# Kernel optimization log

Measured on AMD Instinct MI355X. Metric: run time of the kernel, lower is better.

Reference implementation:

```python
import jax, jax.numpy as jnp
import numpy as np

EPS = 1e-5
C_M = 256
C_Z = 128
C_H = 32  # hardcoded c_hidden in the module


def rms_norm(x, weight, eps=EPS):
    # x * rsqrt(mean(x^2) + eps) * weight over last axis
    ms = jnp.mean(jnp.square(x), axis=-1, keepdims=True)
    return x * jax.lax.rsqrt(ms + eps) * weight


def setup_inputs() -> dict:
    key = jax.random.key(0)
    ks = jax.random.split(key, 8)
    B, S = 256, 384
    m = jax.random.normal(ks[0], (B, S, C_M), dtype=jnp.float32)
    g_in = jnp.ones((C_M,), dtype=jnp.float32)
    Wq = jax.random.normal(ks[1], (C_M, C_H), dtype=jnp.float32) / np.sqrt(C_M)
    bq = jnp.zeros((C_H,), dtype=jnp.float32)
    Wk = jax.random.normal(ks[2], (C_M, C_H), dtype=jnp.float32) / np.sqrt(C_M)
    bk = jnp.zeros((C_H,), dtype=jnp.float32)
    # init='final' means zero-init in AF-style code, but use small random so grads flow
    Wo = jax.random.normal(ks[3], (C_H * C_H, C_Z), dtype=jnp.float32) * 0.02
    bo = jnp.zeros((C_Z,), dtype=jnp.float32)
    g_out = jnp.ones((C_Z,), dtype=jnp.float32)
    return {"m": m, "g_in": g_in, "Wq": Wq, "bq": bq, "Wk": Wk, "bk": bk,
            "Wo": Wo, "bo": bo, "g_out": g_out}


def reference(m, g_in, Wq, bq, Wk, bk, Wo, bo, g_out):
    B, S, _ = m.shape
    m_norm = rms_norm(m, g_in)                       # [B,S,c_m]
    q = m_norm @ Wq + bq                             # [B,S,c_h]
    k = m_norm @ Wk + bk                             # [B,S,c_h]
    # einsum 'bic,bjd->ijcd': sum over MSA depth b
    outer = jnp.einsum('bic,bjd->ijcd', q, k).reshape(S, S, C_H * C_H)
    z = outer @ Wo + bo                              # [S,S,c_z]
    z = rms_norm(z, g_out)
    return z.astype(jnp.float32)
```

## Files before the change

kernel.cpp:

```cpp
#include <hip/hip_runtime.h>
#include <hip/hip_bf16.h>
#include <stdint.h>

#define S   384
#define CM  256
#define CH  32
#define CZ  128
#define BB  256
#define EPS 1e-5f

typedef __attribute__((ext_vector_type(8))) short bf16x8;
typedef __attribute__((ext_vector_type(4))) float f32x4;

#define OFF_QT    0u
#define OFF_KT    6291456u
#define OFF_WT    (OFF_KT + 6291456u)
#define OFF_WOT   (OFF_WT + 32768u)

__device__ __forceinline__ unsigned short f2bf(float x) {
  union { __hip_bfloat16 h; unsigned short u; } v;
  v.h = __float2bfloat16(x);
  return v.u;
}

__device__ __forceinline__ void gload_lds16(const void* g, char* smem, uint32_t lds_off_uniform) {
  uint32_t l32 = (uint32_t)(uintptr_t)(smem + lds_off_uniform);
  __builtin_amdgcn_global_load_lds(
      (const __attribute__((address_space(1))) uint32_t*)(uintptr_t)g,
      (__attribute__((address_space(3))) uint32_t*)(uintptr_t)l32,
      16, 0, 0);
}

__device__ __forceinline__ int olds_off(int ij, int blk) {
  int slot = (blk & ~7) | (((blk & 7) ^ ((blk >> 3) & 7) ^ (ij & 7)) & 7);
  return ij * 2048 + slot * 16;
}

__global__ void k0_prep(const float* __restrict__ Wq, const float* __restrict__ Wk,
                        const float* __restrict__ Wo,
                        unsigned short* __restrict__ WTg, unsigned short* __restrict__ WoTg) {
  int idx = blockIdx.x * 256 + threadIdx.x;
  if (idx < 64 * 256) {
    int c = idx >> 8, t = idx & 255;
    float v = (c < 32) ? Wq[t * 32 + c] : Wk[t * 32 + (c - 32)];
    WTg[c * 256 + t] = f2bf(v);
  }
  int j = idx - 64 * 256;
  if (j >= 0 && j < 128 * 1024) {
    int e = j >> 10, dc = j & 1023;
    int c = dc & 31, d = dc >> 5;
    WoTg[e * 1024 + dc] = f2bf(Wo[(c * 32 + d) * 128 + e]);
  }
}

__global__ __launch_bounds__(256, 2) void k2_proj(const float* __restrict__ m,
                                                  const float* __restrict__ gin,
                                                  const unsigned short* __restrict__ WTg,
                                                  const float* __restrict__ bq,
                                                  const float* __restrict__ bk,
                                                  unsigned short* __restrict__ qT,
                                                  unsigned short* __restrict__ kT) {
  __shared__ char smem[49664 + 18432] __attribute__((aligned(16)));
  const int tid = threadIdx.x;
  const int w = tid >> 6, lane = tid & 63;
  const int mlo = lane & 15, quad = lane >> 4;
  const int i0 = blockIdx.x * 4, b0 = blockIdx.y * 32;
  float* scl = (float*)(smem + 49152);

  #pragma unroll
  for (int s = 0; s < 8; ++s) {
    int C0 = (w * 8 + s) * 2;
    int c = C0 + (lane >> 5);
    int j = lane & 31;
    int t8 = (j & ~7) | ((j & 7) ^ (c & 7));
    gload_lds16(WTg + c * 256 + t8 * 8, smem, 16384u + (uint32_t)C0 * 512u);
  }

  const int rowA = tid >> 1, halfA = tid & 1;
  const int growA = (b0 + (rowA >> 2)) * S + i0 + (rowA & 3);
  {
    const float4* p = (const float4*)(m + (size_t)growA * CM + halfA * 128);
    float ss = 0.f;
    #pragma unroll 8
    for (int q4 = 0; q4 < 32; ++q4) {
      float4 x = p[q4];
      ss += x.x * x.x + x.y * x.y + x.z * x.z + x.w * x.w;
    }
    ss += __shfl_xor(ss, 1, 64);
    if (!halfA) scl[rowA] = rsqrtf(ss * (1.f / 256.f) + EPS);
  }

  f32x4 acc[2][4];
  #pragma unroll
  for (int p = 0; p < 2; ++p)
    #pragma unroll
    for (int q = 0; q < 4; ++q) acc[p][q] = (f32x4)0.f;

  for (int kb = 0; kb < 4; ++kb) {
    __syncthreads();
    {
      const int row = tid >> 1, tk0 = (tid & 1) * 32;
      const float4* pB = (const float4*)(m + (size_t)growA * CM + kb * 64 + tk0);
      const float4* pG = (const float4*)(gin + kb * 64 + tk0);
      float sc = scl[row];
      #pragma unroll
      for (int u = 0; u < 4; ++u) {
        float4 x0 = pB[u * 2], x1 = pB[u * 2 + 1];
        float4 g0 = pG[u * 2], g1 = pG[u * 2 + 1];
        union { unsigned short h[8]; int4 q; } pk;
        pk.h[0] = f2bf(x0.x * sc * g0.x); pk.h[1] = f2bf(x0.y * sc * g0.y);
        pk.h[2] = f2bf(x0.z * sc * g0.z); pk.h[3] = f2bf(x0.w * sc * g0.w);
        pk.h[4] = f2bf(x1.x * sc * g1.x); pk.h[5] = f2bf(x1.y * sc * g1.y);
        pk.h[6] = f2bf(x1.z * sc * g1.z); pk.h[7] = f2bf(x1.w * sc * g1.w);
        int blkid = (((tid & 1) * 4 + u) ^ (row & 7));
        *(int4*)(smem + row * 128 + blkid * 16) = pk.q;
      }
    }
    __syncthreads();
    #pragma unroll
    for (int ks = 0; ks < 2; ++ks) {
      bf16x8 af[2], bfr[4];
      int k8 = ks * 4 + quad;
      #pragma unroll
      for (int fm = 0; fm < 2; ++fm) {
        int mm = w * 32 + fm * 16 + mlo;
        af[fm] = *(const bf16x8*)(smem + mm * 128 + ((k8 ^ (mm & 7)) * 16));
      }
      #pragma unroll
      for (int fn = 0; fn < 4; ++fn) {
        int c = fn * 16 + mlo;
        int t8 = kb * 8 + ks * 4 + quad;
        bfr[fn] = *(const bf16x8*)(smem + 16384 + c * 512 + (((t8 & ~7) | ((t8 & 7) ^ (c & 7))) * 16));
      }
      #pragma unroll
      for (int fm = 0; fm < 2; ++fm)
        #pragma unroll
        for (int fn = 0; fn < 4; ++fn)
          acc[fm][fn] = __builtin_amdgcn_mfma_f32_16x16x32_bf16(af[fm], bfr[fn], acc[fm][fn], 0, 0, 0);
    }
  }
  __syncthreads();
  unsigned short* Cl = (unsigned short*)(smem + 49664);
  #pragma unroll
  for (int fm = 0; fm < 2; ++fm)
    #pragma unroll
    for (int fn = 0; fn < 4; ++fn) {
      int cc = fn * 16 + mlo;
      float bias = (cc < 32) ? bq[cc] : bk[cc - 32];
      #pragma unroll
      for (int r = 0; r < 4; ++r) {
        int rr = w * 32 + fm * 16 + quad * 4 + r;
        Cl[rr * 72 + cc] = f2bf(acc[fm][fn][r] + bias);
      }
    }
  __syncthreads();
  {
    int il = tid >> 6, cc = tid & 63;
    unsigned short* dst = (cc < 32) ? (qT + ((i0 + il) * 32 + cc) * BB + b0)
                                    : (kT + ((i0 + il) * 32 + (cc - 32)) * BB + b0);
    #pragma unroll
    for (int v = 0; v < 4; ++v) {
      union { unsigned short h[8]; int4 q; } u;
      #pragma unroll
      for (int x = 0; x < 8; ++x) u.h[x] = Cl[((v * 8 + x) * 4 + il) * 72 + cc];
      *(int4*)(dst + v * 8) = u.q;
    }
  }
}

__global__ __launch_bounds__(512, 2) void k3_fused(const unsigned short* __restrict__ qT,
                                                   const unsigned short* __restrict__ kT,
                                                   const unsigned short* __restrict__ WoTp,
                                                   const float* __restrict__ bo,
                                                   const float* __restrict__ gout,
                                                   float* __restrict__ out) {
  __shared__ char smem[65536] __attribute__((aligned(16)));
  const int tid = threadIdx.x;
  const int w = tid >> 6, lane = tid & 63;
  const int wm = w & 3, wn = w >> 2;
  const int mlo = lane & 15, quad = lane >> 4;

  const int bid = blockIdx.x;
  const int xcd = bid & 7, idx = bid >> 3;
  const int ti = idx / 12;
  const int tj = xcd * 12 + (idx % 12);

  f32x4 acc[4][4];
  #pragma unroll
  for (int p = 0; p < 4; ++p)
    #pragma unroll
    for (int q = 0; q < 4; ++q) acc[p][q] = (f32x4)0.f;

  auto stageA = [&](int kb) {
    #pragma unroll
    for (int s = 0; s < 4; ++s) {
      int r = w * 32 + s * 8 + (lane >> 3);
      int k8 = (lane & 7) ^ (r & 7);
      gload_lds16(qT + (ti * 256 + r) * BB + kb * 64 + k8 * 8, smem, (uint32_t)(w * 32 + s * 8) * 128u);
    }
  };
  auto stageB = [&](int kb, int bsel) {
    #pragma unroll
    for (int s = 0; s < 2; ++s) {
      int r = w * 16 + s * 8 + (lane >> 3);
      int k8 = (lane & 7) ^ (r & 7);
      gload_lds16(kT + (tj * 128 + r) * BB + kb * 64 + k8 * 8, smem,
                  32768u + (uint32_t)bsel * 16384u + (uint32_t)(w * 16 + s * 8) * 128u);
    }
  };

  stageA(0); stageB(0, 0);
  __syncthreads();

  for (int kb = 0; kb < 4; ++kb) {
    const int bsel = kb & 1;
    bf16x8 af2[2][4];
    #pragma unroll
    for (int ks = 0; ks < 2; ++ks)
      #pragma unroll
      for (int f = 0; f < 4; ++f) {
        int k8 = ks * 4 + quad;
        int mm = wm * 64 + f * 16 + mlo;
        af2[ks][f] = *(const bf16x8*)(smem + mm * 128 + ((k8 ^ (mm & 7)) * 16));
      }
    __syncthreads();
    if (kb < 3) { stageA(kb + 1); stageB(kb + 1, bsel ^ 1); }
    #pragma unroll
    for (int ks = 0; ks < 2; ++ks) {
      bf16x8 bfr[4];
      int k8 = ks * 4 + quad;
      #pragma unroll
      for (int f = 0; f < 4; ++f) {
        int nn = wn * 64 + f * 16 + mlo;
        bfr[f] = *(const bf16x8*)(smem + 32768 + bsel * 16384 + nn * 128 + ((k8 ^ (nn & 7)) * 16));
      }
      #pragma unroll
      for (int fm = 0; fm < 4; ++fm)
        #pragma unroll
        for (int fn = 0; fn < 4; ++fn)
          acc[fm][fn] = __builtin_amdgcn_mfma_f32_16x16x32_bf16(af2[ks][fm], bfr[fn], acc[fm][fn], 0, 0, 0);
    }
    __syncthreads();
  }

  #pragma unroll
  for (int fm = 0; fm < 4; ++fm)
    #pragma unroll
    for (int fn = 0; fn < 4; ++fn) {
      int col = wn * 64 + fn * 16 + mlo;
      int row0 = wm * 64 + fm * 16 + quad * 4;
      int ij = (row0 >> 5) * 4 + (col >> 5);
      int k20 = (col & 31) * 32 + (row0 & 31);
      int blk = k20 >> 3;
      int off = olds_off(ij, blk) + (k20 & 7) * 2;
      union { unsigned short h[4]; uint2 u; } pk;
      #pragma unroll
      for (int r = 0; r < 4; ++r) pk.h[r] = f2bf(acc[fm][fn][r]);
      *(uint2*)(smem + off) = pk.u;
    }
  __syncthreads();

  const int eg = w >> 1, kh = w & 1;
  const int e0 = eg * 32;
  f32x4 acc2[2][2];
  #pragma unroll
  for (int p = 0; p < 2; ++p)
    #pragma unroll
    for (int q = 0; q < 2; ++q) acc2[p][q] = (f32x4)0.f;

  #pragma unroll 4
  for (int s = 0; s < 16; ++s) {
    int kk = kh * 16 + s;
    int k = kk * 32 + quad * 8;
    int blk = kk * 4 + quad;
    bf16x8 b[2];
    #pragma unroll
    for (int fe = 0; fe < 2; ++fe)
      b[fe] = *(const bf16x8*)(WoTp + (size_t)(e0 + fe * 16 + mlo) * 1024 + k);
    #pragma unroll
    for (int fij = 0; fij < 2; ++fij) {
      int ij = fij * 16 + mlo;
      bf16x8 a = *(const bf16x8*)(smem + olds_off(ij, blk));
      #pragma unroll
      for (int fe = 0; fe < 2; ++fe)
        acc2[fij][fe] = __builtin_amdgcn_mfma_f32_16x16x32_bf16(a, b[fe], acc2[fij][fe], 0, 0, 0);
    }
  }
  __syncthreads();

  float* partf = (float*)smem;
  float* red   = (float*)(smem + 16896);
  float* sclp  = (float*)(smem + 17408);
  if (kh == 1) {
    #pragma unroll
    for (int fij = 0; fij < 2; ++fij)
      #pragma unroll
      for (int fe = 0; fe < 2; ++fe)
        #pragma unroll
        for (int r = 0; r < 4; ++r)
          partf[eg * 1056 + (fij * 16 + quad * 4 + r) * 33 + fe * 16 + mlo] = acc2[fij][fe][r];
  }
  __syncthreads();

  float v[2][2][4];
  if (kh == 0) {
    float bv[2], gv[2];
    #pragma unroll
    for (int fe = 0; fe < 2; ++fe) { bv[fe] = bo[e0 + fe * 16 + mlo]; gv[fe] = gout[e0 + fe * 16 + mlo]; }
    float sq[2][4];
    #pragma unroll
    for (int fij = 0; fij < 2; ++fij)
      #pragma unroll
      for (int r = 0; r < 4; ++r) {
        float t = 0.f;
        #pragma unroll
        for (int fe = 0; fe < 2; ++fe) {
          float x = acc2[fij][fe][r] + partf[eg * 1056 + (fij * 16 + quad * 4 + r) * 33 + fe * 16 + mlo] + bv[fe];
          v[fij][fe][r] = x * gv[fe];
          t += x * x;
        }
        sq[fij][r] = t;
      }
    #pragma unroll
    for (int o = 1; o < 16; o <<= 1)
      #pragma unroll
      for (int fij = 0; fij < 2; ++fij)
        #pragma unroll
        for (int r = 0; r < 4; ++r) sq[fij][r] += __shfl_xor(sq[fij][r], o, 64);
    if (mlo == 0) {
      #pragma unroll
      for (int fij = 0; fij < 2; ++fij)
        #pragma unroll
        for (int r = 0; r < 4; ++r) red[(fij * 16 + quad * 4 + r) * 4 + eg] = sq[fij][r];
    }
  }
  __syncthreads();
  if (tid < 32) {
    float t = red[tid * 4] + red[tid * 4 + 1] + red[tid * 4 + 2] + red[tid * 4 + 3];
    sclp[tid] = rsqrtf(t * (1.f / 128.f) + EPS);
  }
  __syncthreads();
  if (kh == 0) {
    #pragma unroll
    for (int fij = 0; fij < 2; ++fij)
      #pragma unroll
      for (int r = 0; r < 4; ++r) {
        int ij = fij * 16 + quad * 4 + r;
        float sc = sclp[ij];
        int gi = ti * 8 + (ij >> 2), gj = tj * 4 + (ij & 3);
        #pragma unroll
        for (int fe = 0; fe < 2; ++fe)
          out[((size_t)gi * S + gj) * CZ + e0 + fe * 16 + mlo] = v[fij][fe][r] * sc;
      }
  }
}

extern "C" void kernel_launch(void* const* d_in, const int* in_sizes, int n_in,
                              void* d_out, int out_size, void* d_ws, size_t ws_size,
                              hipStream_t stream) {
  const float* m    = (const float*)d_in[0];
  const float* gin  = (const float*)d_in[1];
  const float* Wq   = (const float*)d_in[2];
  const float* bq   = (const float*)d_in[3];
  const float* Wk   = (const float*)d_in[4];
  const float* bk   = (const float*)d_in[5];
  const float* Wo   = (const float*)d_in[6];
  const float* bo   = (const float*)d_in[7];
  const float* gout = (const float*)d_in[8];

  char* ws = (char*)d_ws;
  unsigned short* qT    = (unsigned short*)(ws + OFF_QT);
  unsigned short* kT    = (unsigned short*)(ws + OFF_KT);
  unsigned short* WTg   = (unsigned short*)(ws + OFF_WT);
  unsigned short* WoTp  = (unsigned short*)(ws + OFF_WOT);
  float* out = (float*)d_out;

  hipLaunchKernelGGL(k0_prep, dim3(576), dim3(256), 0, stream, Wq, Wk, Wo, WTg, WoTp);
  hipLaunchKernelGGL(k2_proj, dim3(96, 8), dim3(256), 0, stream, m, gin, WTg, bq, bk, qT, kT);
  hipLaunchKernelGGL(k3_fused, dim3(4608), dim3(512), 0, stream, qT, kT, WoTp, bo, gout, out);
}
```

Baseline: 433.6 us.

## Raise occupancy bounds, reuse LDS for projection output, reorder fused MMA loop

The projection kernel's output staging buffer now aliases the start of shared memory instead of a separate region, shrinking its LDS footprint so launch bounds can request 3 blocks per CU. The fused outer-product kernel requests 4 blocks per CU, and its k-loop is restructured so the first half-K MFMAs run before the barrier and only the second A fragment is held in registers across the barrier. This cuts register pressure so the higher occupancy target can fit. The risk is register spills under the tighter bound, and k3's 64KB static LDS may still cap actual residency below the requested count.

```diff
diff --git a/kernel.cpp b/kernel.cpp
--- a/kernel.cpp
+++ b/kernel.cpp
@@ -53,14 +53,14 @@
   }
 }
 
-__global__ __launch_bounds__(256, 2) void k2_proj(const float* __restrict__ m,
+__global__ __launch_bounds__(256, 3) void k2_proj(const float* __restrict__ m,
                                                   const float* __restrict__ gin,
                                                   const unsigned short* __restrict__ WTg,
                                                   const float* __restrict__ bq,
                                                   const float* __restrict__ bk,
                                                   unsigned short* __restrict__ qT,
                                                   unsigned short* __restrict__ kT) {
-  __shared__ char smem[49664 + 18432] __attribute__((aligned(16)));
+  __shared__ char smem[49664] __attribute__((aligned(16)));
   const int tid = threadIdx.x;
   const int w = tid >> 6, lane = tid & 63;
   const int mlo = lane & 15, quad = lane >> 4;
@@ -140,7 +140,7 @@
     }
   }
   __syncthreads();
-  unsigned short* Cl = (unsigned short*)(smem + 49664);
+  unsigned short* Cl = (unsigned short*)smem;
   #pragma unroll
   for (int fm = 0; fm < 2; ++fm)
     #pragma unroll
@@ -168,7 +168,7 @@
   }
 }
 
-__global__ __launch_bounds__(512, 2) void k3_fused(const unsigned short* __restrict__ qT,
+__global__ __launch_bounds__(512, 4) void k3_fused(const unsigned short* __restrict__ qT,
                                                    const unsigned short* __restrict__ kT,
                                                    const unsigned short* __restrict__ WoTp,
                                                    const float* __restrict__ bo,
@@ -214,32 +214,40 @@
 
   for (int kb = 0; kb < 4; ++kb) {
     const int bsel = kb & 1;
-    bf16x8 af2[2][4];
-    #pragma unroll
-    for (int ks = 0; ks < 2; ++ks)
-      #pragma unroll
-      for (int f = 0; f < 4; ++f) {
-        int k8 = ks * 4 + quad;
-        int mm = wm * 64 + f * 16 + mlo;
-        af2[ks][f] = *(const bf16x8*)(smem + mm * 128 + ((k8 ^ (mm & 7)) * 16));
-      }
+    bf16x8 afr[4], bfr[4];
+    #pragma unroll
+    for (int f = 0; f < 4; ++f) {
+      int mm = wm * 64 + f * 16 + mlo;
+      afr[f] = *(const bf16x8*)(smem + mm * 128 + ((quad ^ (mm & 7)) * 16));
+    }
+    #pragma unroll
+    for (int f = 0; f < 4; ++f) {
+      int nn = wn * 64 + f * 16 + mlo;
+      bfr[f] = *(const bf16x8*)(smem + 32768 + bsel * 16384 + nn * 128 + ((quad ^ (nn & 7)) * 16));
+    }
+    #pragma unroll
+    for (int fm = 0; fm < 4; ++fm)
+      #pragma unroll
+      for (int fn = 0; fn < 4; ++fn)
+        acc[fm][fn] = __builtin_amdgcn_mfma_f32_16x16x32_bf16(afr[fm], bfr[fn], acc[fm][fn], 0, 0, 0);
+    bf16x8 af1[4];
+    #pragma unroll
+    for (int f = 0; f < 4; ++f) {
+      int mm = wm * 64 + f * 16 + mlo;
+      af1[f] = *(const bf16x8*)(smem + mm * 128 + (((4 + quad) ^ (mm & 7)) * 16));
+    }
     __syncthreads();
     if (kb < 3) { stageA(kb + 1); stageB(kb + 1, bsel ^ 1); }
     #pragma unroll
-    for (int ks = 0; ks < 2; ++ks) {
-      bf16x8 bfr[4];
-      int k8 = ks * 4 + quad;
-      #pragma unroll
-      for (int f = 0; f < 4; ++f) {
-        int nn = wn * 64 + f * 16 + mlo;
-        bfr[f] = *(const bf16x8*)(smem + 32768 + bsel * 16384 + nn * 128 + ((k8 ^ (nn & 7)) * 16));
-      }
-      #pragma unroll
-      for (int fm = 0; fm < 4; ++fm)
-        #pragma unroll
-        for (int fn = 0; fn < 4; ++fn)
-          acc[fm][fn] = __builtin_amdgcn_mfma_f32_16x16x32_bf16(af2[ks][fm], bfr[fn], acc[fm][fn], 0, 0, 0);
-    }
+    for (int f = 0; f < 4; ++f) {
+      int nn = wn * 64 + f * 16 + mlo;
+      bfr[f] = *(const bf16x8*)(smem + 32768 + bsel * 16384 + nn * 128 + (((4 + quad) ^ (nn & 7)) * 16));
+    }
+    #pragma unroll
+    for (int fm = 0; fm < 4; ++fm)
+      #pragma unroll
+      for (int fn = 0; fn < 4; ++fn)
+        acc[fm][fn] = __builtin_amdgcn_mfma_f32_16x16x32_bf16(af1[fm], bfr[fn], acc[fm][fn], 0, 0, 0);
     __syncthreads();
   }
 
```

Result: faster. 390.0 us (-10.1%).
